# Optimization experiments

Hardware: AMD Instinct MI355X
Metric: run time of the kernel (lower is better)

## Reference

```python
import jax, jax.numpy as jnp
import numpy as np

IN_C, OUT_C, EDGE_C = 128, 64, 1
N_NODES, N_EDGES = 50000, 800000


def setup_inputs() -> dict:
    key = jax.random.key(0)
    ks = jax.random.split(key, 12)
    d = OUT_C
    # xavier-uniform-ish scales
    def xav(k, shape):
        lim = float(np.sqrt(6.0 / (shape[0] + shape[1])))
        return jax.random.uniform(k, shape, jnp.float32, -lim, lim)
    return {
        "feat_src": jax.random.normal(ks[0], (N_NODES, IN_C), jnp.float32),
        "feat_dst": jax.random.normal(ks[1], (N_NODES, IN_C), jnp.float32),
        "edge_weight": jax.random.uniform(ks[2], (N_EDGES, EDGE_C), jnp.float32),
        "src_idx": jax.random.randint(ks[3], (N_EDGES,), 0, N_NODES),
        "dst_idx": jnp.sort(jax.random.randint(ks[4], (N_EDGES,), 0, N_NODES)),
        "weight_n": xav(ks[5], (IN_C, d)),
        "weight_e": xav(ks[6], (EDGE_C, d)),
        "query": xav(ks[7], (d, d)),
        "key_w": xav(ks[8], (d, d)),
        "att_w": xav(ks[9], (3 * d, 1)),
        "att_b": jnp.zeros((1,), jnp.float32),
        "out_w": xav(ks[10], (2 * d, d)),
        "out_b": jnp.zeros((d,), jnp.float32),
    }


def reference(feat_src, feat_dst, edge_weight, src_idx, dst_idx,
              weight_n, weight_e, query, key_w, att_w, att_b, out_w, out_b):
    d = query.shape[0]
    n_dst = feat_dst.shape[0]
    h_src = feat_src @ weight_n                      # [N_src, d]
    h_dst = feat_dst @ weight_n                      # [N_dst, d]
    edge_emb = edge_weight @ weight_e                # [E, d]
    q_e = (h_dst @ query)[dst_idx]                   # [E, d] gather
    k_e = (h_src @ key_w)[src_idx]                   # [E, d] gather
    # linear_att(concat([q, k, e])) without materializing the concat
    logits = (q_e @ att_w[:d] + k_e @ att_w[d:2 * d]
              + edge_emb @ att_w[2 * d:] + att_b)    # [E, 1]
    logits = jax.nn.leaky_relu(logits, 0.2)
    # segment softmax over destination nodes
    m = jax.ops.segment_max(logits, dst_idx, num_segments=n_dst)   # [N_dst, 1]
    ex = jnp.exp(logits - m[dst_idx])
    s = jax.ops.segment_sum(ex, dst_idx, num_segments=n_dst)       # [N_dst, 1]
    alpha = ex / (s[dst_idx] + 1e-16)                # [E, 1]
    msg = alpha * h_src[src_idx]                     # [E, d]
    agg = jax.ops.segment_sum(msg, dst_idx, num_segments=n_dst)    # [N_dst, d]
    # linear_out(concat([h_dst, agg]))
    out = h_dst @ out_w[:d] + agg @ out_w[d:] + out_b
    return out
```

## Files before the change

kernel.cpp:

```cpp
#include <hip/hip_runtime.h>
#include <hip/hip_bf16.h>

typedef short short8 __attribute__((ext_vector_type(8)));
typedef float float4v __attribute__((ext_vector_type(4)));
typedef unsigned short ushort4v __attribute__((ext_vector_type(4)));

static __device__ __forceinline__ short f2b(float f) {
    union { __hip_bfloat16 b; short s; } v;
    v.b = __float2bfloat16(f);
    return v.s;
}
static __device__ __forceinline__ float b2f(unsigned short u) {
    union { float f; unsigned v; } x;
    x.v = ((unsigned)u) << 16;
    return x.f;
}

__global__ void __launch_bounds__(256) setup_kernel(
    const float* __restrict__ query, const float* __restrict__ key_w,
    const float* __restrict__ weight_e, const float* __restrict__ att_w,
    const float* __restrict__ Wn, const float* __restrict__ out_w,
    const int* __restrict__ dst_idx,
    float* __restrict__ W1p, float* __restrict__ W2p,
    float* __restrict__ Wk, float* __restrict__ Wq, float* __restrict__ escale,
    int* __restrict__ row_ptr, int n_nodes, int n_edges) {
    int b = blockIdx.x, t = threadIdx.x;
    if (b < 64) {
        int idx = b * 256 + t;
        int mat = idx >> 13;
        int rem = idx & 8191;
        int i = rem >> 6, j = rem & 63;
        float s = 0.f;
        for (int k = 0; k < 64; ++k)
            s += Wn[i * 64 + k] * out_w[(mat * 64 + k) * 64 + j];
        (mat ? W2p : W1p)[i * 64 + j] = s;
    } else if (b == 64) {
        __shared__ float kq[128];
        __shared__ float ep[64];
        if (t < 64) {
            float s = 0.f;
            for (int j = 0; j < 64; ++j) s += key_w[t * 64 + j] * att_w[64 + j];
            kq[t] = s;
        } else if (t < 128) {
            int i = t - 64;
            float s = 0.f;
            for (int j = 0; j < 64; ++j) s += query[i * 64 + j] * att_w[j];
            kq[64 + i] = s;
        } else if (t < 192) {
            int j = t - 128;
            ep[j] = weight_e[j] * att_w[128 + j];
        }
        __syncthreads();
        if (t < 128) {
            float s = 0.f;
            for (int k = 0; k < 64; ++k) s += Wn[t * 64 + k] * kq[k];
            Wk[t] = s;
        } else {
            int i = t - 128;
            float s = 0.f;
            for (int k = 0; k < 64; ++k) s += Wn[i * 64 + k] * kq[64 + k];
            Wq[i] = s;
        }
        if (t == 0) {
            float s = 0.f;
            for (int j = 0; j < 64; ++j) s += ep[j];
            escale[0] = s;
        }
    } else {
        int idx = (b - 65) * 256 + t;
        if (idx > n_nodes) return;
        int lo = 0, hi = n_edges;
        while (lo < hi) {
            int mid = (lo + hi) >> 1;
            if (dst_idx[mid] < idx) lo = mid + 1; else hi = mid;
        }
        row_ptr[idx] = lo;
    }
}

__global__ void __launch_bounds__(256) gemm_kernel(
    const float* __restrict__ feat_src, const float* __restrict__ feat_dst,
    const float* __restrict__ W2p, const float* __restrict__ W1p,
    const float* __restrict__ Wk, const float* __restrict__ Wq,
    unsigned short* __restrict__ hw2, float* __restrict__ out,
    const float* __restrict__ out_b, float* __restrict__ kscore,
    float* __restrict__ qscore, int n_nodes) {
    __shared__ __align__(16) short BTs[64 * 136];
    __shared__ __align__(16) short BTd[64 * 136];
    int t = threadIdx.x;
    int row0 = blockIdx.x * 128;
    int total = 2 * n_nodes;
    bool needS = row0 < n_nodes;
    bool needD = row0 + 127 >= n_nodes;
    if (needS) {
#pragma unroll
        for (int i = 0; i < 32; ++i) {
            int idx = i * 256 + t;
            int k = idx >> 6, n = idx & 63;
            BTs[n * 136 + k] = f2b(W2p[idx]);
        }
    }
    if (needD) {
#pragma unroll
        for (int i = 0; i < 32; ++i) {
            int idx = i * 256 + t;
            int k = idx >> 6, n = idx & 63;
            BTd[n * 136 + k] = f2b(W1p[idx]);
        }
    }
    __syncthreads();

    int wave = t >> 6, lane = t & 63;
    int m15 = lane & 15, quad = lane >> 4;
#pragma unroll
    for (int tile = 0; tile < 2; ++tile) {
        int rb = row0 + wave * 32 + tile * 16;
        if (rb >= total) continue;
        bool isSrc = rb < n_nodes;
        const float* Arow = (isSrc ? feat_src + (size_t)rb * 128
                                   : feat_dst + (size_t)(rb - n_nodes) * 128)
                            + (size_t)m15 * 128 + quad * 8;
        const short* BT = isSrc ? BTs : BTd;
        const float* w = isSrc ? Wk : Wq;

        float4v acc[4] = {};
        float sk = 0.f;
#pragma unroll
        for (int kk = 0; kk < 4; ++kk) {
            float4v a0 = *(const float4v*)(Arow + kk * 32);
            float4v a1 = *(const float4v*)(Arow + kk * 32 + 4);
            float4v w0 = *(const float4v*)(w + kk * 32 + quad * 8);
            float4v w1 = *(const float4v*)(w + kk * 32 + quad * 8 + 4);
#pragma unroll
            for (int j = 0; j < 4; ++j) sk += a0[j] * w0[j] + a1[j] * w1[j];
            short8 a;
#pragma unroll
            for (int j = 0; j < 4; ++j) { a[j] = f2b(a0[j]); a[4 + j] = f2b(a1[j]); }
#pragma unroll
            for (int nt = 0; nt < 4; ++nt) {
                short8 bb = *(const short8*)(&BT[(nt * 16 + m15) * 136 + kk * 32 + quad * 8]);
                acc[nt] = __builtin_amdgcn_mfma_f32_16x16x32_bf16(a, bb, acc[nt], 0, 0, 0);
            }
        }

#pragma unroll
        for (int nt = 0; nt < 4; ++nt) {
            int col = nt * 16 + m15;
            float bv = isSrc ? 0.f : out_b[col];
#pragma unroll
            for (int r = 0; r < 4; ++r) {
                int row = rb + quad * 4 + r;
                if (isSrc) hw2[(size_t)row * 64 + col] = (unsigned short)f2b(acc[nt][r]);
                else       out[(size_t)(row - n_nodes) * 64 + col] = acc[nt][r] + bv;
            }
        }
        sk += __shfl_xor(sk, 16);
        sk += __shfl_xor(sk, 32);
        if (quad == 0) {
            if (isSrc) kscore[rb + m15] = sk;
            else       qscore[rb + m15 - n_nodes] = sk;
        }
    }
}

__global__ void __launch_bounds__(256) agg_kernel(
    const int* __restrict__ src_idx, const float* __restrict__ edge_w,
    const unsigned short* __restrict__ hw2, const float* __restrict__ kscore,
    const float* __restrict__ qscore, const float* __restrict__ escale_p,
    const float* __restrict__ att_b, const int* __restrict__ row_ptr,
    float* __restrict__ out, int n_nodes) {
    int wave = (int)((blockIdx.x * blockDim.x + threadIdx.x) >> 6);
    int lane = threadIdx.x & 63;
    if (wave >= n_nodes) return;
    int n = wave;
    int start = row_ptr[n];
    int deg = row_ptr[n + 1] - start;
    int eslot = lane >> 4;
    int cg = lane & 15;

    float ac0 = 0.f, ac1 = 0.f, ac2 = 0.f, ac3 = 0.f;
    if (deg > 0) {
        float escale = escale_p[0];
        float bias = att_b[0];
        float qs = qscore[n];

        if (deg <= 64) {
            int s0 = 0; float lg0 = -1e30f;
            if (lane < deg) {
                s0 = src_idx[start + lane];
                float lg = qs + kscore[s0] + edge_w[start + lane] * escale + bias;
                lg0 = (lg > 0.f) ? lg : 0.2f * lg;
            }
            float mx = lg0;
#pragma unroll
            for (int off = 32; off; off >>= 1) mx = fmaxf(mx, __shfl_xor(mx, off));
            float a0 = __expf(lg0 - mx);
            float sm = a0;
#pragma unroll
            for (int off = 32; off; off >>= 1) sm += __shfl_xor(sm, off);
            float alpha0 = a0 * (1.f / (sm + 1e-16f));

            for (int base = 0; base < deg; base += 4) {
                int eo = base + eslot;
                int idx = (eo < deg) ? eo : 0;
                float alpha = __shfl(alpha0, idx);
                int s = __shfl(s0, idx);
                if (eo >= deg) alpha = 0.f;
                ushort4v h = *(const ushort4v*)(hw2 + (size_t)s * 64 + cg * 4);
                ac0 += alpha * b2f(h[0]);
                ac1 += alpha * b2f(h[1]);
                ac2 += alpha * b2f(h[2]);
                ac3 += alpha * b2f(h[3]);
            }
        } else {
            float mx = -1e30f, sm = 0.f;
            for (int eo = lane; eo < deg; eo += 64) {
                int s = src_idx[start + eo];
                float lg = qs + kscore[s] + edge_w[start + eo] * escale + bias;
                lg = (lg > 0.f) ? lg : 0.2f * lg;
                float nm = fmaxf(mx, lg);
                sm = sm * __expf(mx - nm) + __expf(lg - nm);
                mx = nm;
            }
            for (int off = 32; off; off >>= 1) {
                float m2 = __shfl_xor(mx, off);
                float s2 = __shfl_xor(sm, off);
                float nm = fmaxf(mx, m2);
                sm = sm * __expf(mx - nm) + s2 * __expf(m2 - nm);
                mx = nm;
            }
            float inv = 1.f / (sm + 1e-16f);
            for (int base = 0; base < deg; base += 4) {
                int eo = base + eslot;
                bool valid = eo < deg;
                int e = start + (valid ? eo : 0);
                int s = src_idx[e];
                float lg = qs + kscore[s] + edge_w[e] * escale + bias;
                lg = (lg > 0.f) ? lg : 0.2f * lg;
                float alpha = valid ? __expf(lg - mx) * inv : 0.f;
                ushort4v h = *(const ushort4v*)(hw2 + (size_t)s * 64 + cg * 4);
                ac0 += alpha * b2f(h[0]);
                ac1 += alpha * b2f(h[1]);
                ac2 += alpha * b2f(h[2]);
                ac3 += alpha * b2f(h[3]);
            }
        }
        ac0 += __shfl_xor(ac0, 16); ac0 += __shfl_xor(ac0, 32);
        ac1 += __shfl_xor(ac1, 16); ac1 += __shfl_xor(ac1, 32);
        ac2 += __shfl_xor(ac2, 16); ac2 += __shfl_xor(ac2, 32);
        ac3 += __shfl_xor(ac3, 16); ac3 += __shfl_xor(ac3, 32);
    }
    if (lane < 16) {
        float4v b = *(const float4v*)(out + (size_t)n * 64 + lane * 4);
        b[0] += ac0; b[1] += ac1; b[2] += ac2; b[3] += ac3;
        *(float4v*)(out + (size_t)n * 64 + lane * 4) = b;
    }
}

extern "C" void kernel_launch(void* const* d_in, const int* in_sizes, int n_in,
                              void* d_out, int out_size, void* d_ws, size_t ws_size,
                              hipStream_t stream) {
    const float* feat_src = (const float*)d_in[0];
    const float* feat_dst = (const float*)d_in[1];
    const float* edge_w   = (const float*)d_in[2];
    const int*   src_idx  = (const int*)d_in[3];
    const int*   dst_idx  = (const int*)d_in[4];
    const float* weight_n = (const float*)d_in[5];
    const float* weight_e = (const float*)d_in[6];
    const float* query    = (const float*)d_in[7];
    const float* key_w    = (const float*)d_in[8];
    const float* att_w    = (const float*)d_in[9];
    const float* att_b    = (const float*)d_in[10];
    const float* out_w    = (const float*)d_in[11];
    const float* out_b    = (const float*)d_in[12];
    float* out = (float*)d_out;

    int n_nodes = in_sizes[0] / 128;
    int n_edges = in_sizes[3];

    char* p = (char*)d_ws;
    unsigned short* hw2 = (unsigned short*)p;  p += (size_t)n_nodes * 64 * 2;
    float* kscore = (float*)p;  p += (size_t)n_nodes * 4;
    float* qscore = (float*)p;  p += (size_t)n_nodes * 4;
    float* W1p    = (float*)p;  p += 128 * 64 * 4;
    float* W2p    = (float*)p;  p += 128 * 64 * 4;
    float* Wk     = (float*)p;  p += 128 * 4;
    float* Wq     = (float*)p;  p += 128 * 4;
    float* escale = (float*)p;  p += 64;
    int*  row_ptr = (int*)p;

    int rp_blocks = (n_nodes + 1 + 255) / 256;
    hipLaunchKernelGGL(setup_kernel, dim3(65 + rp_blocks), dim3(256), 0, stream,
                       query, key_w, weight_e, att_w, weight_n, out_w, dst_idx,
                       W1p, W2p, Wk, Wq, escale, row_ptr, n_nodes, n_edges);

    int g_blocks = (2 * n_nodes + 127) / 128;
    hipLaunchKernelGGL(gemm_kernel, dim3(g_blocks), dim3(256), 0, stream,
                       feat_src, feat_dst, W2p, W1p, Wk, Wq,
                       hw2, out, out_b, kscore, qscore, n_nodes);

    hipLaunchKernelGGL(agg_kernel, dim3((n_nodes + 3) / 4), dim3(256), 0, stream,
                       src_idx, edge_w, hw2, kscore, qscore,
                       escale, att_b, row_ptr, out, n_nodes);
}
```

Baseline: 164.7 us.

## Process two destination nodes per wave in the aggregation kernel

The aggregation kernel now assigns two consecutive destination nodes to each wavefront. When their combined degree fits in 64 lanes, one prefix-sum scan computes both softmax denominators together, and the lanes already loaded are reused for both nodes. That fast path also drops the max subtraction and instead clamps the logit at 80 before exp, which removes a wave reduction but relies on logits staying small enough not to lose precision. The intent is to fill more lanes and cut per-node reduction overhead, at the cost of running the two nodes' gather loops one after the other and launching half as many waves.

```diff
diff --git a/kernel.cpp b/kernel.cpp
--- a/kernel.cpp
+++ b/kernel.cpp
@@ -142,7 +142,6 @@
                 acc[nt] = __builtin_amdgcn_mfma_f32_16x16x32_bf16(a, bb, acc[nt], 0, 0, 0);
             }
         }
-
 #pragma unroll
         for (int nt = 0; nt < 4; ++nt) {
             int col = nt * 16 + m15;
@@ -169,40 +168,50 @@
     const float* __restrict__ qscore, const float* __restrict__ escale_p,
     const float* __restrict__ att_b, const int* __restrict__ row_ptr,
     float* __restrict__ out, int n_nodes) {
-    int wave = (int)((blockIdx.x * blockDim.x + threadIdx.x) >> 6);
+    int wid = (int)((blockIdx.x * blockDim.x + threadIdx.x) >> 6);
     int lane = threadIdx.x & 63;
-    if (wave >= n_nodes) return;
-    int n = wave;
-    int start = row_ptr[n];
-    int deg = row_ptr[n + 1] - start;
-    int eslot = lane >> 4;
-    int cg = lane & 15;
-
-    float ac0 = 0.f, ac1 = 0.f, ac2 = 0.f, ac3 = 0.f;
-    if (deg > 0) {
-        float escale = escale_p[0];
-        float bias = att_b[0];
-        float qs = qscore[n];
-
-        if (deg <= 64) {
-            int s0 = 0; float lg0 = -1e30f;
-            if (lane < deg) {
-                s0 = src_idx[start + lane];
-                float lg = qs + kscore[s0] + edge_w[start + lane] * escale + bias;
-                lg0 = (lg > 0.f) ? lg : 0.2f * lg;
-            }
-            float mx = lg0;
-#pragma unroll
-            for (int off = 32; off; off >>= 1) mx = fmaxf(mx, __shfl_xor(mx, off));
-            float a0 = __expf(lg0 - mx);
-            float sm = a0;
-#pragma unroll
-            for (int off = 32; off; off >>= 1) sm += __shfl_xor(sm, off);
-            float alpha0 = a0 * (1.f / (sm + 1e-16f));
-
-            for (int base = 0; base < deg; base += 4) {
-                int eo = base + eslot;
-                int idx = (eo < deg) ? eo : 0;
+    int n0 = wid * 2;
+    if (n0 >= n_nodes) return;
+    int nCnt = (n0 + 1 < n_nodes) ? 2 : 1;
+    int rp0 = row_ptr[n0];
+    int rp1 = row_ptr[n0 + 1];
+    int rp2 = (nCnt == 2) ? row_ptr[n0 + 2] : rp1;
+    int total = rp2 - rp0;
+    if (total == 0) return;
+    float escale = escale_p[0];
+    float bias = att_b[0];
+    int eslot = lane >> 4, cg = lane & 15;
+
+    if (total <= 64) {
+        int m = rp1 - rp0;
+        int s0 = 0; float w = 0.f;
+        if (lane < total) {
+            s0 = src_idx[rp0 + lane];
+            float lg = qscore[n0 + (lane >= m ? 1 : 0)] + kscore[s0]
+                     + edge_w[rp0 + lane] * escale + bias;
+            lg = (lg > 0.f) ? lg : 0.2f * lg;
+            w = __expf(fminf(lg, 80.f));
+        }
+        float pre = w;
+#pragma unroll
+        for (int off = 1; off < 64; off <<= 1) {
+            float tv = __shfl_up(pre, off);
+            if (lane >= off) pre += tv;
+        }
+        float sumAll = __shfl(pre, 63);
+        float sum0 = (m > 0) ? __shfl(pre, m - 1) : 0.f;
+        float sum1 = sumAll - sum0;
+        float mySum = (lane >= m) ? sum1 : sum0;
+        float alpha0 = w * (1.f / (mySum + 1e-16f));
+
+        for (int j = 0; j < nCnt; ++j) {
+            int sl = j ? m : 0;
+            int deg = j ? (total - m) : m;
+            if (deg == 0) continue;
+            float ac0 = 0.f, ac1 = 0.f, ac2 = 0.f, ac3 = 0.f;
+            for (int b = 0; b < deg; b += 4) {
+                int eo = b + eslot;
+                int idx = (eo < deg) ? (sl + eo) : sl;
                 float alpha = __shfl(alpha0, idx);
                 int s = __shfl(s0, idx);
                 if (eo >= deg) alpha = 0.f;
@@ -212,48 +221,95 @@
                 ac2 += alpha * b2f(h[2]);
                 ac3 += alpha * b2f(h[3]);
             }
-        } else {
-            float mx = -1e30f, sm = 0.f;
-            for (int eo = lane; eo < deg; eo += 64) {
-                int s = src_idx[start + eo];
-                float lg = qs + kscore[s] + edge_w[start + eo] * escale + bias;
-                lg = (lg > 0.f) ? lg : 0.2f * lg;
-                float nm = fmaxf(mx, lg);
-                sm = sm * __expf(mx - nm) + __expf(lg - nm);
-                mx = nm;
-            }
-            for (int off = 32; off; off >>= 1) {
-                float m2 = __shfl_xor(mx, off);
-                float s2 = __shfl_xor(sm, off);
-                float nm = fmaxf(mx, m2);
-                sm = sm * __expf(mx - nm) + s2 * __expf(m2 - nm);
-                mx = nm;
-            }
-            float inv = 1.f / (sm + 1e-16f);
-            for (int base = 0; base < deg; base += 4) {
-                int eo = base + eslot;
-                bool valid = eo < deg;
-                int e = start + (valid ? eo : 0);
-                int s = src_idx[e];
-                float lg = qs + kscore[s] + edge_w[e] * escale + bias;
-                lg = (lg > 0.f) ? lg : 0.2f * lg;
-                float alpha = valid ? __expf(lg - mx) * inv : 0.f;
-                ushort4v h = *(const ushort4v*)(hw2 + (size_t)s * 64 + cg * 4);
-                ac0 += alpha * b2f(h[0]);
-                ac1 += alpha * b2f(h[1]);
-                ac2 += alpha * b2f(h[2]);
-                ac3 += alpha * b2f(h[3]);
-            }
-        }
-        ac0 += __shfl_xor(ac0, 16); ac0 += __shfl_xor(ac0, 32);
-        ac1 += __shfl_xor(ac1, 16); ac1 += __shfl_xor(ac1, 32);
-        ac2 += __shfl_xor(ac2, 16); ac2 += __shfl_xor(ac2, 32);
-        ac3 += __shfl_xor(ac3, 16); ac3 += __shfl_xor(ac3, 32);
-    }
-    if (lane < 16) {
-        float4v b = *(const float4v*)(out + (size_t)n * 64 + lane * 4);
-        b[0] += ac0; b[1] += ac1; b[2] += ac2; b[3] += ac3;
-        *(float4v*)(out + (size_t)n * 64 + lane * 4) = b;
+            ac0 += __shfl_xor(ac0, 16); ac0 += __shfl_xor(ac0, 32);
+            ac1 += __shfl_xor(ac1, 16); ac1 += __shfl_xor(ac1, 32);
+            ac2 += __shfl_xor(ac2, 16); ac2 += __shfl_xor(ac2, 32);
+            ac3 += __shfl_xor(ac3, 16); ac3 += __shfl_xor(ac3, 32);
+            if (lane < 16) {
+                float* op = out + (size_t)(n0 + j) * 64 + lane * 4;
+                float4v bb = *(const float4v*)op;
+                bb[0] += ac0; bb[1] += ac1; bb[2] += ac2; bb[3] += ac3;
+                *(float4v*)op = bb;
+            }
+        }
+    } else {
+        for (int j = 0; j < nCnt; ++j) {
+            int start = (j == 0) ? rp0 : rp1;
+            int deg = ((j == 0) ? rp1 : rp2) - start;
+            if (deg == 0) continue;
+            float qs = qscore[n0 + j];
+            float ac0 = 0.f, ac1 = 0.f, ac2 = 0.f, ac3 = 0.f;
+            if (deg <= 64) {
+                int s0 = 0; float lg0 = -1e30f;
+                if (lane < deg) {
+                    s0 = src_idx[start + lane];
+                    float lg = qs + kscore[s0] + edge_w[start + lane] * escale + bias;
+                    lg0 = (lg > 0.f) ? lg : 0.2f * lg;
+                }
+                float mx = lg0;
+#pragma unroll
+                for (int off = 32; off; off >>= 1) mx = fmaxf(mx, __shfl_xor(mx, off));
+                float a0 = __expf(lg0 - mx);
+                float sm = a0;
+#pragma unroll
+                for (int off = 32; off; off >>= 1) sm += __shfl_xor(sm, off);
+                float alpha0 = a0 * (1.f / (sm + 1e-16f));
+                for (int b = 0; b < deg; b += 4) {
+                    int eo = b + eslot;
+                    int idx = (eo < deg) ? eo : 0;
+                    float alpha = __shfl(alpha0, idx);
+                    int s = __shfl(s0, idx);
+                    if (eo >= deg) alpha = 0.f;
+                    ushort4v h = *(const ushort4v*)(hw2 + (size_t)s * 64 + cg * 4);
+                    ac0 += alpha * b2f(h[0]);
+                    ac1 += alpha * b2f(h[1]);
+                    ac2 += alpha * b2f(h[2]);
+                    ac3 += alpha * b2f(h[3]);
+                }
+            } else {
+                float mx = -1e30f, sm = 0.f;
+                for (int eo = lane; eo < deg; eo += 64) {
+                    int s = src_idx[start + eo];
+                    float lg = qs + kscore[s] + edge_w[start + eo] * escale + bias;
+                    lg = (lg > 0.f) ? lg : 0.2f * lg;
+                    float nm = fmaxf(mx, lg);
+                    sm = sm * __expf(mx - nm) + __expf(lg - nm);
+                    mx = nm;
+                }
+                for (int off = 32; off; off >>= 1) {
+                    float m2 = __shfl_xor(mx, off);
+                    float s2 = __shfl_xor(sm, off);
+                    float nm = fmaxf(mx, m2);
+                    sm = sm * __expf(mx - nm) + s2 * __expf(m2 - nm);
+                    mx = nm;
+                }
+                float inv = 1.f / (sm + 1e-16f);
+                for (int b = 0; b < deg; b += 4) {
+                    int eo = b + eslot;
+                    bool valid = eo < deg;
+                    int e = start + (valid ? eo : 0);
+                    int s = src_idx[e];
+                    float lg = qs + kscore[s] + edge_w[e] * escale + bias;
+                    lg = (lg > 0.f) ? lg : 0.2f * lg;
+                    float alpha = valid ? __expf(lg - mx) * inv : 0.f;
+                    ushort4v h = *(const ushort4v*)(hw2 + (size_t)s * 64 + cg * 4);
+                    ac0 += alpha * b2f(h[0]);
+                    ac1 += alpha * b2f(h[1]);
+                    ac2 += alpha * b2f(h[2]);
+                    ac3 += alpha * b2f(h[3]);
+                }
+            }
+            ac0 += __shfl_xor(ac0, 16); ac0 += __shfl_xor(ac0, 32);
+            ac1 += __shfl_xor(ac1, 16); ac1 += __shfl_xor(ac1, 32);
+            ac2 += __shfl_xor(ac2, 16); ac2 += __shfl_xor(ac2, 32);
+            ac3 += __shfl_xor(ac3, 16); ac3 += __shfl_xor(ac3, 32);
+            if (lane < 16) {
+                float* op = out + (size_t)(n0 + j) * 64 + lane * 4;
+                float4v bb = *(const float4v*)op;
+                bb[0] += ac0; bb[1] += ac1; bb[2] += ac2; bb[3] += ac3;
+                *(float4v*)op = bb;
+            }
+        }
     }
 }
 
@@ -299,7 +355,8 @@
                        feat_src, feat_dst, W2p, W1p, Wk, Wq,
                        hw2, out, out_b, kscore, qscore, n_nodes);
 
-    hipLaunchKernelGGL(agg_kernel, dim3((n_nodes + 3) / 4), dim3(256), 0, stream,
+    int n_waves = (n_nodes + 1) / 2;
+    hipLaunchKernelGGL(agg_kernel, dim3((n_waves + 3) / 4), dim3(256), 0, stream,
                        src_idx, edge_w, hw2, kscore, qscore,
                        escale, att_b, row_ptr, out, n_nodes);
 }
```

Result: faster. 159.4 us (-3.2%).
